# Kernel optimization log

Measured on AMD Instinct MI355X. Metric: run time of the kernel, lower is better.

The kernel has to match this reference:

```python
import jax, jax.numpy as jnp
import numpy as np

N, D, H, E, K = 8192, 1024, 2048, 8, 2

def setup_inputs() -> dict:
    key = jax.random.key(0)
    ks = jax.random.split(key, 8)
    x = jax.random.normal(ks[0], (N, D), dtype=jnp.float32)
    # Expert params stacked over the expert axis (E, ...)
    W1 = jax.random.normal(ks[1], (E, D, H), dtype=jnp.float32) * (1.0 / np.sqrt(D))
    b1 = jnp.zeros((E, H), dtype=jnp.float32)
    W2 = jax.random.normal(ks[2], (E, H, D), dtype=jnp.float32) * (1.0 / np.sqrt(H))
    b2 = jnp.zeros((E, D), dtype=jnp.float32)
    # Gating linear
    Wg = jax.random.normal(ks[3], (D, E), dtype=jnp.float32) * (1.0 / np.sqrt(D))
    bg = jnp.zeros((E,), dtype=jnp.float32)
    # Externalized gating noise (torch uses randn_like(logits) * 0.1)
    noise = jax.random.normal(ks[4], (N, E), dtype=jnp.float32)
    return {"x": x, "W1": W1, "b1": b1, "W2": W2, "b2": b2, "Wg": Wg, "bg": bg, "noise": noise}


def reference(x, W1, b1, W2, b2, Wg, bg, noise):
    n = x.shape[0]
    # --- gating: noisy top-k + softmax over top-k, scattered to dense weights ---
    logits = x @ Wg + bg                                  # [N, E]
    noisy = logits + 0.1 * noise
    top_v, top_i = jax.lax.top_k(noisy, K)                # [N, K]
    w = jax.nn.softmax(top_v, axis=-1)                    # [N, K]
    rows = jnp.arange(n)[:, None]
    sparse_w = jnp.zeros_like(logits).at[rows, top_i].set(w)  # [N, E]
    # --- all experts on all tokens (faithful to the dense-stack implementation) ---
    h = jax.nn.relu(jnp.einsum('nd,edh->neh', x, W1) + b1)    # [N, E, H]
    expert_out = jnp.einsum('neh,ehd->ned', h, W2) + b2       # [N, E, D]
    # --- weighted combine ---
    return jnp.einsum('ne,ned->nd', sparse_w, expert_out)     # [N, D]
```

## Files before the change

kernel.cpp:

```cpp
#include <hip/hip_runtime.h>
#include <stdint.h>
#include <stddef.h>

#define NTOK 8192
#define DDIM 1024
#define HDIM 2048
#define NEXP 8
#define GROWS 16384

typedef __attribute__((ext_vector_type(8))) short short8;
typedef __attribute__((ext_vector_type(8))) unsigned short ushort8;
typedef __attribute__((ext_vector_type(4))) float floatx4;

#define AS1 __attribute__((address_space(1)))
#define AS3 __attribute__((address_space(3)))

#define MAXRT 136
#define MAXT1 (MAXRT * (HDIM / 128))
#define MAXT2 (MAXRT * (DDIM / 128))

constexpr size_t OFF_CNT  = 0;
constexpr size_t OFF_TB1  = 256;
constexpr size_t OFF_TB2  = OFF_TB1 + 8960;
constexpr size_t OFF_TKI  = OFF_TB2 + 4608;
constexpr size_t OFF_TKW  = OFF_TKI + (size_t)NTOK * 8;
constexpr size_t OFF_LIST = OFF_TKW + (size_t)NTOK * 8;
constexpr size_t OFF_WTS  = OFF_LIST + (size_t)NEXP * NTOK * 4;
constexpr size_t OFF_XBF  = OFF_WTS + (size_t)NEXP * NTOK * 4;
constexpr size_t OFF_AKB  = OFF_XBF + (size_t)NTOK * DDIM * 2;
constexpr size_t OFF_W1KB = OFF_AKB + (size_t)GROWS * DDIM * 2;
constexpr size_t OFF_W2KB = OFF_W1KB + (size_t)NEXP * DDIM * HDIM * 2;
constexpr size_t OFF_HKB  = OFF_W2KB + (size_t)NEXP * DDIM * HDIM * 2;

__device__ __forceinline__ unsigned short f2bf(float f) {
  union { float f; unsigned u; } v; v.f = f;
  unsigned r = v.u + 0x7FFFu + ((v.u >> 16) & 1u);
  return (unsigned short)(r >> 16);
}

__global__ __launch_bounds__(256) void gate_kernel(
    const float* __restrict__ x, const float* __restrict__ Wg,
    const float* __restrict__ bg, const float* __restrict__ noise,
    int2* __restrict__ tki, float2* __restrict__ tkw,
    unsigned short* __restrict__ xbf) {
  int lane = threadIdx.x & 63;
  int wid  = threadIdx.x >> 6;
  int token = blockIdx.x * 4 + wid;
  const float* xr = x + (size_t)token * DDIM;
  unsigned short* xo = xbf + (size_t)token * DDIM;
  double acc[NEXP];
#pragma unroll
  for (int e = 0; e < NEXP; ++e) acc[e] = 0.0;
  for (int d = lane; d < DDIM; d += 64) {
    float xv = xr[d];
    xo[d] = f2bf(xv);
    const floatx4* wp = (const floatx4*)(Wg + d * NEXP);
    floatx4 w0 = wp[0], w1 = wp[1];
#pragma unroll
    for (int j = 0; j < 4; ++j) {
      acc[j]     += (double)xv * (double)w0[j];
      acc[4 + j] += (double)xv * (double)w1[j];
    }
  }
#pragma unroll
  for (int e = 0; e < NEXP; ++e)
#pragma unroll
    for (int off = 32; off > 0; off >>= 1) acc[e] += __shfl_xor(acc[e], off);
  if (lane == 0) {
    float nv[NEXP];
#pragma unroll
    for (int e = 0; e < NEXP; ++e) {
      float lg = (float)(acc[e] + (double)bg[e]);
      nv[e] = lg + 0.1f * noise[token * NEXP + e];
    }
    int i1 = 0; float v1 = nv[0];
#pragma unroll
    for (int e = 1; e < NEXP; ++e) if (nv[e] > v1) { v1 = nv[e]; i1 = e; }
    int i2 = -1; float v2 = -3.4e38f;
#pragma unroll
    for (int e = 0; e < NEXP; ++e) if (e != i1 && nv[e] > v2) { v2 = nv[e]; i2 = e; }
    float tt  = expf(v2 - v1);
    tki[token] = make_int2(i1, i2);
    tkw[token] = make_float2(1.0f / (1.0f + tt), tt / (1.0f + tt));
  }
}

__global__ __launch_bounds__(256) void scatter_kernel(
    const int2* __restrict__ tki, const float2* __restrict__ tkw,
    int* __restrict__ counts, int* __restrict__ lists, float* __restrict__ wts) {
  int e = blockIdx.x;
  int tid = threadIdx.x;
  int lane = tid & 63, wid = tid >> 6;
  __shared__ int wave_cnt[4];
  __shared__ int run_total;
  if (tid == 0) run_total = 0;
  __syncthreads();
  for (int t0 = 0; t0 < NTOK; t0 += 256) {
    int tok = t0 + tid;
    int2 ki = tki[tok];
    float2 kw = tkw[tok];
    bool sel = (ki.x == e) || (ki.y == e);
    float w = (ki.x == e) ? kw.x : kw.y;
    unsigned long long mask = __ballot(sel);
    int pos = __popcll(mask & ((1ull << lane) - 1ull));
    if (lane == 0) wave_cnt[wid] = __popcll(mask);
    __syncthreads();
    int base = run_total;
    for (int i = 0; i < wid; ++i) base += wave_cnt[i];
    if (sel) {
      lists[e * NTOK + base + pos] = tok;
      wts[e * NTOK + base + pos] = w;
    }
    __syncthreads();
    if (tid == 0) run_total += wave_cnt[0] + wave_cnt[1] + wave_cnt[2] + wave_cnt[3];
    __syncthreads();
  }
  if (tid == 0) counts[e] = run_total;
}

__global__ __launch_bounds__(256) void gather_a_kernel(
    const unsigned short* __restrict__ xbf, const int* __restrict__ counts,
    const int* __restrict__ lists, unsigned short* __restrict__ akb) {
  int kt   = blockIdx.y;
  int grow = blockIdx.x * 256 + threadIdx.x;
  int c[8];
#pragma unroll
  for (int i = 0; i < 8; ++i) c[i] = counts[i];
  int e = 0, off = 0;
#pragma unroll
  for (int i = 0; i < 8; ++i)
    if (e == i && grow >= off + c[i]) { off += c[i]; e = i + 1; }
  int tok = lists[e * NTOK + (grow - off)];
  const ushort8* s = (const ushort8*)(xbf + (size_t)tok * DDIM + kt * 32);
  ushort8* d = (ushort8*)(akb + (size_t)kt * GROWS * 32 + (size_t)grow * 32);
  d[0] = s[0]; d[1] = s[1]; d[2] = s[2]; d[3] = s[3];
}

__global__ __launch_bounds__(256) void build_tiles_kernel(
    const int* __restrict__ counts, int* __restrict__ tb1, int* __restrict__ tb2) {
  int tid = threadIdx.x;
  int ct[8], cum[9];
  cum[0] = 0;
#pragma unroll
  for (int e = 0; e < 8; ++e) { ct[e] = (counts[e] + 127) >> 7; cum[e + 1] = cum[e] + ct[e]; }
  int nt = cum[8];
  constexpr int NBY1 = HDIM / 128, NBY2 = DDIM / 128;
  if (tid == 0) { tb1[0] = nt * NBY1; tb2[0] = nt * NBY2; }
  for (int idx = tid; idx < nt * NBY1; idx += 256) {
    int e = 0;
    while (idx >= cum[e + 1] * NBY1) ++e;
    int r = idx - cum[e] * NBY1;
    int by = r / ct[e], bx = r - by * ct[e];
    tb1[1 + idx] = (e << 16) | (bx << 8) | by;
  }
  for (int idx = tid; idx < nt * NBY2; idx += 256) {
    int e = 0;
    while (idx >= cum[e + 1] * NBY2) ++e;
    int r = idx - cum[e] * NBY2;
    int by = r / ct[e], bx = r - by * ct[e];
    tb2[1 + idx] = (e << 16) | (bx << 8) | by;
  }
}

__global__ __launch_bounds__(256) void transpose_cvt_kernel(
    const float* __restrict__ W, unsigned short* __restrict__ WT, int R, int C) {
  __shared__ float tile[64][65];
  int e = blockIdx.z;
  const float* Win = W + (size_t)e * R * C;
  unsigned short* Wout = WT + (size_t)e * R * C;
  int c0 = blockIdx.x * 64, r0 = blockIdx.y * 64;
  int tx = threadIdx.x & 63, ty = threadIdx.x >> 6;
#pragma unroll
  for (int i = ty; i < 64; i += 4)
    tile[i][tx] = Win[(size_t)(r0 + i) * C + c0 + tx];
  __syncthreads();
  int cc = threadIdx.x >> 2, seg = (threadIdx.x & 3) * 16;
  ushort8 o0, o1;
#pragma unroll
  for (int j = 0; j < 8; ++j) o0[j] = f2bf(tile[seg + j][cc]);
#pragma unroll
  for (int j = 0; j < 8; ++j) o1[j] = f2bf(tile[seg + 8 + j][cc]);
  int koff = r0 + seg;
  unsigned short* outp = Wout + (size_t)(koff >> 5) * C * 32
                              + (size_t)(c0 + cc) * 32 + (koff & 31);
  *(ushort8*)(outp) = o0;
  *(ushort8*)(outp + 8) = o1;
}

template <int KDIM, int NDIM, bool IS_G1>
__global__ __launch_bounds__(256) void moe_gemm_kernel(
    const unsigned short* __restrict__ Akb,
    const unsigned short* __restrict__ Bkb,
    const float* __restrict__ bias,
    const int* __restrict__ counts, const int* __restrict__ lists,
    const float* __restrict__ wts, const int* __restrict__ tbl,
    unsigned short* __restrict__ Hkb,
    float* __restrict__ Out) {
  __shared__ __align__(16) char smem[32768];
  constexpr int NT = KDIM / 32;
  constexpr size_t A_KT = (size_t)GROWS * 32;
  constexpr size_t B_KT = (size_t)NDIM * 32;

  int ntiles = tbl[0];
  int bid = blockIdx.x;
  if (bid >= ntiles) return;
  int q = ntiles >> 3, rr = ntiles & 7;
  int xcd = bid & 7, within = bid >> 3;
  int widx = (xcd < rr ? xcd * (q + 1) : rr * (q + 1) + (xcd - rr) * q) + within;
  int desc = tbl[1 + widx];
  int e  = desc >> 16;
  int bx = (desc >> 8) & 0xff;
  int by = desc & 0xff;

  int Me, off_e = 0;
  {
    int c[8];
#pragma unroll
    for (int i = 0; i < 8; ++i) c[i] = counts[i];
    Me = c[e];
#pragma unroll
    for (int i = 0; i < 8; ++i) if (i < e) off_e += c[i];
  }

  int tid = threadIdx.x;
  int lane = tid & 63, wid = tid >> 6;
  int wr = wid >> 1, wc = wid & 1;
  int r16 = lane & 15, g4 = lane >> 4;

  int r0 = tid >> 2;
  int ch = ((tid & 3) ^ ((r0 >> 1) & 3)) * 8;
  const unsigned short *sA0, *sA1, *sB0, *sB1;
  {
    int lr0 = bx * 128 + r0, lr1 = lr0 + 64;
    int g0 = off_e + (lr0 < Me ? lr0 : 0);
    int g1 = off_e + (lr1 < Me ? lr1 : 0);
    sA0 = Akb + (size_t)g0 * 32 + ch;
    sA1 = Akb + (size_t)g1 * 32 + ch;
    const unsigned short* be = Bkb + (size_t)e * KDIM * NDIM;
    sB0 = be + (size_t)(by * 128 + r0) * 32 + ch;
    sB1 = be + (size_t)(by * 128 + 64 + r0) * 32 + ch;
  }

  auto stage = [&](int t) {
    int buf = t & 1;
    char* da = smem + buf * 8192 + tid * 16;
    char* db = smem + 16384 + buf * 8192 + tid * 16;
    size_t ao = (size_t)t * A_KT, bo = (size_t)t * B_KT;
    __builtin_amdgcn_global_load_lds((const AS1 void*)(sA0 + ao), (AS3 void*)da, 16, 0, 0);
    __builtin_amdgcn_global_load_lds((const AS1 void*)(sA1 + ao), (AS3 void*)(da + 4096), 16, 0, 0);
    __builtin_amdgcn_global_load_lds((const AS1 void*)(sB0 + bo), (AS3 void*)db, 16, 0, 0);
    __builtin_amdgcn_global_load_lds((const AS1 void*)(sB1 + bo), (AS3 void*)(db + 4096), 16, 0, 0);
  };

  int aoff[4], boff[4];
#pragma unroll
  for (int m = 0; m < 4; ++m) {
    int rowa = wr * 64 + m * 16 + r16;
    aoff[m] = rowa * 64 + ((g4 ^ ((rowa >> 1) & 3)) * 16);
  }
#pragma unroll
  for (int n = 0; n < 4; ++n) {
    int rowb = wc * 64 + n * 16 + r16;
    boff[n] = 16384 + rowb * 64 + ((g4 ^ ((rowb >> 1) & 3)) * 16);
  }

  floatx4 acc[4][4];
#pragma unroll
  for (int m = 0; m < 4; ++m)
#pragma unroll
    for (int n = 0; n < 4; ++n) acc[m][n] = (floatx4){0.f, 0.f, 0.f, 0.f};

  stage(0);
  stage(1);

  for (int t = 0; t < NT; ++t) {
    if (t + 1 < NT) { asm volatile("s_waitcnt vmcnt(4)" ::: "memory"); }
    else            { asm volatile("s_waitcnt vmcnt(0)" ::: "memory"); }
    __builtin_amdgcn_s_barrier();
    __builtin_amdgcn_sched_barrier(0);
    const char* pa = smem + (t & 1) * 8192;
    const char* pb = smem + (t & 1) * 8192;
    short8 a[4], b[4];
#pragma unroll
    for (int m = 0; m < 4; ++m) a[m] = *(const short8*)(pa + aoff[m]);
#pragma unroll
    for (int n = 0; n < 4; ++n) b[n] = *(const short8*)(pb + boff[n]);
#pragma unroll
    for (int m = 0; m < 4; ++m)
#pragma unroll
      for (int n = 0; n < 4; ++n)
        acc[m][n] = __builtin_amdgcn_mfma_f32_16x16x32_bf16(a[m], b[n], acc[m][n], 0, 0, 0);
    __builtin_amdgcn_s_barrier();
    __builtin_amdgcn_sched_barrier(0);
    if (t + 2 < NT) stage(t + 2);
  }

  if constexpr (IS_G1) {
#pragma unroll
    for (int m = 0; m < 4; ++m) {
#pragma unroll
      for (int i = 0; i < 4; ++i) {
        int lrow = bx * 128 + wr * 64 + m * 16 + g4 * 4 + i;
        if (lrow < Me) {
          size_t grow = (size_t)(off_e + lrow);
#pragma unroll
          for (int n = 0; n < 4; ++n) {
            int col = by * 128 + wc * 64 + n * 16 + r16;
            float v = acc[m][n][i] + bias[e * NDIM + col];
            Hkb[(size_t)(col >> 5) * A_KT + grow * 32 + (col & 31)] = f2bf(fmaxf(v, 0.f));
          }
        }
      }
    }
  } else {
#pragma unroll
    for (int m = 0; m < 4; ++m) {
#pragma unroll
      for (int i = 0; i < 4; ++i) {
        int lrow = bx * 128 + wr * 64 + m * 16 + g4 * 4 + i;
        if (lrow < Me) {
          int tok = lists[e * NTOK + lrow];
          float w = wts[e * NTOK + lrow];
          float* orow = Out + (size_t)tok * NDIM + by * 128;
#pragma unroll
          for (int n = 0; n < 4; ++n) {
            int col = wc * 64 + n * 16 + r16;
            float v = acc[m][n][i] + bias[e * NDIM + by * 128 + col];
            atomicAdd(orow + col, w * v);
          }
        }
      }
    }
  }
}

extern "C" void kernel_launch(void* const* d_in, const int* in_sizes, int n_in,
                              void* d_out, int out_size, void* d_ws, size_t ws_size,
                              hipStream_t stream) {
  (void)in_sizes; (void)n_in; (void)ws_size;
  const float* x     = (const float*)d_in[0];
  const float* W1    = (const float*)d_in[1];
  const float* b1    = (const float*)d_in[2];
  const float* W2    = (const float*)d_in[3];
  const float* b2    = (const float*)d_in[4];
  const float* Wg    = (const float*)d_in[5];
  const float* bg    = (const float*)d_in[6];
  const float* noise = (const float*)d_in[7];
  float* out = (float*)d_out;

  char* ws = (char*)d_ws;
  int*            counts = (int*)(ws + OFF_CNT);
  int*            tb1    = (int*)(ws + OFF_TB1);
  int*            tb2    = (int*)(ws + OFF_TB2);
  int2*           tki    = (int2*)(ws + OFF_TKI);
  float2*         tkw    = (float2*)(ws + OFF_TKW);
  int*            lists  = (int*)(ws + OFF_LIST);
  float*          wts    = (float*)(ws + OFF_WTS);
  unsigned short* xbf    = (unsigned short*)(ws + OFF_XBF);
  unsigned short* akb    = (unsigned short*)(ws + OFF_AKB);
  unsigned short* w1kb   = (unsigned short*)(ws + OFF_W1KB);
  unsigned short* w2kb   = (unsigned short*)(ws + OFF_W2KB);
  unsigned short* hkb    = (unsigned short*)(ws + OFF_HKB);

  hipMemsetAsync(d_out, 0, (size_t)out_size * sizeof(float), stream);
  hipMemsetAsync(counts, 0, 256, stream);

  gate_kernel<<<NTOK / 4, 256, 0, stream>>>(x, Wg, bg, noise, tki, tkw, xbf);
  scatter_kernel<<<NEXP, 256, 0, stream>>>(tki, tkw, counts, lists, wts);
  build_tiles_kernel<<<1, 256, 0, stream>>>(counts, tb1, tb2);
  gather_a_kernel<<<dim3(GROWS / 256, DDIM / 32), 256, 0, stream>>>(xbf, counts, lists, akb);
  transpose_cvt_kernel<<<dim3(HDIM / 64, DDIM / 64, NEXP), 256, 0, stream>>>(W1, w1kb, DDIM, HDIM);
  transpose_cvt_kernel<<<dim3(DDIM / 64, HDIM / 64, NEXP), 256, 0, stream>>>(W2, w2kb, HDIM, DDIM);

  moe_gemm_kernel<DDIM, HDIM, true>
      <<<MAXT1, 256, 0, stream>>>(akb, w1kb, b1, counts, lists, wts, tb1, hkb, nullptr);
  moe_gemm_kernel<HDIM, DDIM, false>
      <<<MAXT2, 256, 0, stream>>>(hkb, w2kb, b2, counts, lists, wts, tb2, nullptr, out);
}
```

Before: 366.6 us.

## Enlarge MoE GEMM tiles to 256 rows and split-K the second GEMM

Each GEMM block now handles a pair of 128-row tiles (256 rows) that share one loaded B tile, so B traffic from global memory per output is roughly halved. LDS rises to 48KB and each wave holds two accumulator sets. The second GEMM also splits K in two, recovering block count, and adds the bias only in the first K half. The cost is more register pressure and lower occupancy, plus twice as many atomic adds in the second GEMM's output.

```diff
diff --git a/kernel.cpp b/kernel.cpp
--- a/kernel.cpp
+++ b/kernel.cpp
@@ -15,14 +15,13 @@
 #define AS1 __attribute__((address_space(1)))
 #define AS3 __attribute__((address_space(3)))
 
-#define MAXRT 136
-#define MAXT1 (MAXRT * (HDIM / 128))
-#define MAXT2 (MAXRT * (DDIM / 128))
+#define MAXT1 (72 * (HDIM / 128))
+#define MAXT2 (72 * (DDIM / 128) * 2)
 
 constexpr size_t OFF_CNT  = 0;
 constexpr size_t OFF_TB1  = 256;
-constexpr size_t OFF_TB2  = OFF_TB1 + 8960;
-constexpr size_t OFF_TKI  = OFF_TB2 + 4608;
+constexpr size_t OFF_TB2  = OFF_TB1 + 4864;
+constexpr size_t OFF_TKI  = OFF_TB2 + 4864;
 constexpr size_t OFF_TKW  = OFF_TKI + (size_t)NTOK * 8;
 constexpr size_t OFF_LIST = OFF_TKW + (size_t)NTOK * 8;
 constexpr size_t OFF_WTS  = OFF_LIST + (size_t)NEXP * NTOK * 4;
@@ -139,26 +138,31 @@
 __global__ __launch_bounds__(256) void build_tiles_kernel(
     const int* __restrict__ counts, int* __restrict__ tb1, int* __restrict__ tb2) {
   int tid = threadIdx.x;
-  int ct[8], cum[9];
+  int pr[8], cum[9];
   cum[0] = 0;
 #pragma unroll
-  for (int e = 0; e < 8; ++e) { ct[e] = (counts[e] + 127) >> 7; cum[e + 1] = cum[e] + ct[e]; }
-  int nt = cum[8];
+  for (int e = 0; e < 8; ++e) {
+    int ct = (counts[e] + 127) >> 7;
+    pr[e] = (ct + 1) >> 1;
+    cum[e + 1] = cum[e] + pr[e];
+  }
+  int np = cum[8];
   constexpr int NBY1 = HDIM / 128, NBY2 = DDIM / 128;
-  if (tid == 0) { tb1[0] = nt * NBY1; tb2[0] = nt * NBY2; }
-  for (int idx = tid; idx < nt * NBY1; idx += 256) {
+  if (tid == 0) { tb1[0] = np * NBY1; tb2[0] = np * NBY2 * 2; }
+  for (int idx = tid; idx < np * NBY1; idx += 256) {
     int e = 0;
     while (idx >= cum[e + 1] * NBY1) ++e;
     int r = idx - cum[e] * NBY1;
-    int by = r / ct[e], bx = r - by * ct[e];
-    tb1[1 + idx] = (e << 16) | (bx << 8) | by;
-  }
-  for (int idx = tid; idx < nt * NBY2; idx += 256) {
+    int by = r / pr[e], p = r - by * pr[e];
+    tb1[1 + idx] = (e << 16) | (p << 8) | by;
+  }
+  for (int idx = tid; idx < np * NBY2 * 2; idx += 256) {
     int e = 0;
-    while (idx >= cum[e + 1] * NBY2) ++e;
-    int r = idx - cum[e] * NBY2;
-    int by = r / ct[e], bx = r - by * ct[e];
-    tb2[1 + idx] = (e << 16) | (bx << 8) | by;
+    while (idx >= cum[e + 1] * NBY2 * 2) ++e;
+    int r = idx - cum[e] * NBY2 * 2;
+    int khby = r / pr[e], p = r - khby * pr[e];
+    int kh = khby / NBY2, by = khby - kh * NBY2;
+    tb2[1 + idx] = (kh << 24) | (e << 16) | (p << 8) | by;
   }
 }
 
@@ -187,7 +191,7 @@
   *(ushort8*)(outp + 8) = o1;
 }
 
-template <int KDIM, int NDIM, bool IS_G1>
+template <int KDIM, int NDIM, int KSPLIT, bool IS_G1>
 __global__ __launch_bounds__(256) void moe_gemm_kernel(
     const unsigned short* __restrict__ Akb,
     const unsigned short* __restrict__ Bkb,
@@ -196,8 +200,9 @@
     const float* __restrict__ wts, const int* __restrict__ tbl,
     unsigned short* __restrict__ Hkb,
     float* __restrict__ Out) {
-  __shared__ __align__(16) char smem[32768];
-  constexpr int NT = KDIM / 32;
+  __shared__ __align__(16) char smem[49152];
+  constexpr int KLEN = KDIM / KSPLIT;
+  constexpr int NT = KLEN / 32;
   constexpr size_t A_KT = (size_t)GROWS * 32;
   constexpr size_t B_KT = (size_t)NDIM * 32;
 
@@ -208,9 +213,11 @@
   int xcd = bid & 7, within = bid >> 3;
   int widx = (xcd < rr ? xcd * (q + 1) : rr * (q + 1) + (xcd - rr) * q) + within;
   int desc = tbl[1 + widx];
-  int e  = desc >> 16;
-  int bx = (desc >> 8) & 0xff;
+  int kh = (desc >> 24) & 1;
+  int e  = (desc >> 16) & 0xff;
+  int p  = (desc >> 8) & 0xff;
   int by = desc & 0xff;
+  int bx0 = 2 * p, bx1 = 2 * p + 1;
 
   int Me, off_e = 0;
   {
@@ -221,6 +228,7 @@
 #pragma unroll
     for (int i = 0; i < 8; ++i) if (i < e) off_e += c[i];
   }
+  bool has1 = (bx1 * 128 < Me);
 
   int tid = threadIdx.x;
   int lane = tid & 63, wid = tid >> 6;
@@ -229,27 +237,36 @@
 
   int r0 = tid >> 2;
   int ch = ((tid & 3) ^ ((r0 >> 1) & 3)) * 8;
-  const unsigned short *sA0, *sA1, *sB0, *sB1;
+  int ktbase = kh * NT;
+  const unsigned short *sA[2][2], *sB[2];
+#pragma unroll
+  for (int tt = 0; tt < 2; ++tt) {
+    int bxx = tt ? bx1 : bx0;
+#pragma unroll
+    for (int i = 0; i < 2; ++i) {
+      int lr = bxx * 128 + i * 64 + r0;
+      int g = off_e + (lr < Me ? lr : 0);
+      sA[tt][i] = Akb + (size_t)ktbase * A_KT + (size_t)g * 32 + ch;
+    }
+  }
   {
-    int lr0 = bx * 128 + r0, lr1 = lr0 + 64;
-    int g0 = off_e + (lr0 < Me ? lr0 : 0);
-    int g1 = off_e + (lr1 < Me ? lr1 : 0);
-    sA0 = Akb + (size_t)g0 * 32 + ch;
-    sA1 = Akb + (size_t)g1 * 32 + ch;
-    const unsigned short* be = Bkb + (size_t)e * KDIM * NDIM;
-    sB0 = be + (size_t)(by * 128 + r0) * 32 + ch;
-    sB1 = be + (size_t)(by * 128 + 64 + r0) * 32 + ch;
+    const unsigned short* be = Bkb + (size_t)e * KDIM * NDIM + (size_t)ktbase * B_KT;
+    sB[0] = be + (size_t)(by * 128 + r0) * 32 + ch;
+    sB[1] = be + (size_t)(by * 128 + 64 + r0) * 32 + ch;
   }
 
   auto stage = [&](int t) {
     int buf = t & 1;
-    char* da = smem + buf * 8192 + tid * 16;
-    char* db = smem + 16384 + buf * 8192 + tid * 16;
+    char* da0 = smem + buf * 8192 + tid * 16;
+    char* da1 = smem + 16384 + buf * 8192 + tid * 16;
+    char* db  = smem + 32768 + buf * 8192 + tid * 16;
     size_t ao = (size_t)t * A_KT, bo = (size_t)t * B_KT;
-    __builtin_amdgcn_global_load_lds((const AS1 void*)(sA0 + ao), (AS3 void*)da, 16, 0, 0);
-    __builtin_amdgcn_global_load_lds((const AS1 void*)(sA1 + ao), (AS3 void*)(da + 4096), 16, 0, 0);
-    __builtin_amdgcn_global_load_lds((const AS1 void*)(sB0 + bo), (AS3 void*)db, 16, 0, 0);
-    __builtin_amdgcn_global_load_lds((const AS1 void*)(sB1 + bo), (AS3 void*)(db + 4096), 16, 0, 0);
+    __builtin_amdgcn_global_load_lds((const AS1 void*)(sA[0][0] + ao), (AS3 void*)da0, 16, 0, 0);
+    __builtin_amdgcn_global_load_lds((const AS1 void*)(sA[0][1] + ao), (AS3 void*)(da0 + 4096), 16, 0, 0);
+    __builtin_amdgcn_global_load_lds((const AS1 void*)(sA[1][0] + ao), (AS3 void*)da1, 16, 0, 0);
+    __builtin_amdgcn_global_load_lds((const AS1 void*)(sA[1][1] + ao), (AS3 void*)(da1 + 4096), 16, 0, 0);
+    __builtin_amdgcn_global_load_lds((const AS1 void*)(sB[0] + bo),  (AS3 void*)db, 16, 0, 0);
+    __builtin_amdgcn_global_load_lds((const AS1 void*)(sB[1] + bo),  (AS3 void*)(db + 4096), 16, 0, 0);
   };
 
   int aoff[4], boff[4];
@@ -261,35 +278,44 @@
 #pragma unroll
   for (int n = 0; n < 4; ++n) {
     int rowb = wc * 64 + n * 16 + r16;
-    boff[n] = 16384 + rowb * 64 + ((g4 ^ ((rowb >> 1) & 3)) * 16);
-  }
-
-  floatx4 acc[4][4];
+    boff[n] = 32768 + rowb * 64 + ((g4 ^ ((rowb >> 1) & 3)) * 16);
+  }
+
+  floatx4 acc0[4][4], acc1[4][4];
 #pragma unroll
   for (int m = 0; m < 4; ++m)
 #pragma unroll
-    for (int n = 0; n < 4; ++n) acc[m][n] = (floatx4){0.f, 0.f, 0.f, 0.f};
+    for (int n = 0; n < 4; ++n) {
+      acc0[m][n] = (floatx4){0.f, 0.f, 0.f, 0.f};
+      acc1[m][n] = (floatx4){0.f, 0.f, 0.f, 0.f};
+    }
 
   stage(0);
   stage(1);
 
   for (int t = 0; t < NT; ++t) {
-    if (t + 1 < NT) { asm volatile("s_waitcnt vmcnt(4)" ::: "memory"); }
+    if (t + 1 < NT) { asm volatile("s_waitcnt vmcnt(6)" ::: "memory"); }
     else            { asm volatile("s_waitcnt vmcnt(0)" ::: "memory"); }
     __builtin_amdgcn_s_barrier();
     __builtin_amdgcn_sched_barrier(0);
-    const char* pa = smem + (t & 1) * 8192;
-    const char* pb = smem + (t & 1) * 8192;
-    short8 a[4], b[4];
-#pragma unroll
-    for (int m = 0; m < 4; ++m) a[m] = *(const short8*)(pa + aoff[m]);
+    const char* pa0 = smem + (t & 1) * 8192;
+    const char* pa1 = smem + 16384 + (t & 1) * 8192;
+    const char* pb  = smem + (t & 1) * 8192;
+    short8 a0[4], a1[4], b[4];
+#pragma unroll
+    for (int m = 0; m < 4; ++m) {
+      a0[m] = *(const short8*)(pa0 + aoff[m]);
+      a1[m] = *(const short8*)(pa1 + aoff[m]);
+    }
 #pragma unroll
     for (int n = 0; n < 4; ++n) b[n] = *(const short8*)(pb + boff[n]);
 #pragma unroll
     for (int m = 0; m < 4; ++m)
 #pragma unroll
-      for (int n = 0; n < 4; ++n)
-        acc[m][n] = __builtin_amdgcn_mfma_f32_16x16x32_bf16(a[m], b[n], acc[m][n], 0, 0, 0);
+      for (int n = 0; n < 4; ++n) {
+        acc0[m][n] = __builtin_amdgcn_mfma_f32_16x16x32_bf16(a0[m], b[n], acc0[m][n], 0, 0, 0);
+        acc1[m][n] = __builtin_amdgcn_mfma_f32_16x16x32_bf16(a1[m], b[n], acc1[m][n], 0, 0, 0);
+      }
     __builtin_amdgcn_s_barrier();
     __builtin_amdgcn_sched_barrier(0);
     if (t + 2 < NT) stage(t + 2);
@@ -300,24 +326,42 @@
     for (int m = 0; m < 4; ++m) {
 #pragma unroll
       for (int i = 0; i < 4; ++i) {
-        int lrow = bx * 128 + wr * 64 + m * 16 + g4 * 4 + i;
+        int lrow = bx0 * 128 + wr * 64 + m * 16 + g4 * 4 + i;
         if (lrow < Me) {
           size_t grow = (size_t)(off_e + lrow);
 #pragma unroll
           for (int n = 0; n < 4; ++n) {
             int col = by * 128 + wc * 64 + n * 16 + r16;
-            float v = acc[m][n][i] + bias[e * NDIM + col];
+            float v = acc0[m][n][i] + bias[e * NDIM + col];
             Hkb[(size_t)(col >> 5) * A_KT + grow * 32 + (col & 31)] = f2bf(fmaxf(v, 0.f));
           }
         }
       }
     }
+    if (has1) {
+#pragma unroll
+      for (int m = 0; m < 4; ++m) {
+#pragma unroll
+        for (int i = 0; i < 4; ++i) {
+          int lrow = bx1 * 128 + wr * 64 + m * 16 + g4 * 4 + i;
+          if (lrow < Me) {
+            size_t grow = (size_t)(off_e + lrow);
+#pragma unroll
+            for (int n = 0; n < 4; ++n) {
+              int col = by * 128 + wc * 64 + n * 16 + r16;
+              float v = acc1[m][n][i] + bias[e * NDIM + col];
+              Hkb[(size_t)(col >> 5) * A_KT + grow * 32 + (col & 31)] = f2bf(fmaxf(v, 0.f));
+            }
+          }
+        }
+      }
+    }
   } else {
 #pragma unroll
     for (int m = 0; m < 4; ++m) {
 #pragma unroll
       for (int i = 0; i < 4; ++i) {
-        int lrow = bx * 128 + wr * 64 + m * 16 + g4 * 4 + i;
+        int lrow = bx0 * 128 + wr * 64 + m * 16 + g4 * 4 + i;
         if (lrow < Me) {
           int tok = lists[e * NTOK + lrow];
           float w = wts[e * NTOK + lrow];
@@ -325,8 +369,28 @@
 #pragma unroll
           for (int n = 0; n < 4; ++n) {
             int col = wc * 64 + n * 16 + r16;
-            float v = acc[m][n][i] + bias[e * NDIM + by * 128 + col];
+            float v = acc0[m][n][i] + (kh == 0 ? bias[e * NDIM + by * 128 + col] : 0.f);
             atomicAdd(orow + col, w * v);
+          }
+        }
+      }
+    }
+    if (has1) {
+#pragma unroll
+      for (int m = 0; m < 4; ++m) {
+#pragma unroll
+        for (int i = 0; i < 4; ++i) {
+          int lrow = bx1 * 128 + wr * 64 + m * 16 + g4 * 4 + i;
+          if (lrow < Me) {
+            int tok = lists[e * NTOK + lrow];
+            float w = wts[e * NTOK + lrow];
+            float* orow = Out + (size_t)tok * NDIM + by * 128;
+#pragma unroll
+            for (int n = 0; n < 4; ++n) {
+              int col = wc * 64 + n * 16 + r16;
+              float v = acc1[m][n][i] + (kh == 0 ? bias[e * NDIM + by * 128 + col] : 0.f);
+              atomicAdd(orow + col, w * v);
+            }
           }
         }
       }
@@ -372,8 +436,8 @@
   transpose_cvt_kernel<<<dim3(HDIM / 64, DDIM / 64, NEXP), 256, 0, stream>>>(W1, w1kb, DDIM, HDIM);
   transpose_cvt_kernel<<<dim3(DDIM / 64, HDIM / 64, NEXP), 256, 0, stream>>>(W2, w2kb, HDIM, DDIM);
 
-  moe_gemm_kernel<DDIM, HDIM, true>
+  moe_gemm_kernel<DDIM, HDIM, 1, true>
       <<<MAXT1, 256, 0, stream>>>(akb, w1kb, b1, counts, lists, wts, tb1, hkb, nullptr);
-  moe_gemm_kernel<HDIM, DDIM, false>
+  moe_gemm_kernel<HDIM, DDIM, 2, false>
       <<<MAXT2, 256, 0, stream>>>(hkb, w2kb, b2, counts, lists, wts, tb2, nullptr, out);
 }
```

Result: slower. 656.8 us (+79.2%).
